# Optimization experiments

Hardware: AMD Instinct MI355X
Metric: run time of the kernel (lower is better)

Reference implementation:

```python
import jax, jax.numpy as jnp
import numpy as np

D_MODEL = 1024
NUM_HEADS = 16
D_K = D_MODEL // NUM_HEADS
TEMPERATURE = 1.0
EPS = 1e-6


def setup_inputs() -> dict:
    key = jax.random.key(0)
    ks = jax.random.split(key, 8)
    B, S, D, H = 2, 2048, D_MODEL, NUM_HEADS
    sc = 1.0 / np.sqrt(D)
    x = jax.random.normal(ks[0], (B, S, D), dtype=jnp.float32)
    Wq = jax.random.normal(ks[1], (D, D), dtype=jnp.float32) * sc
    Wk = jax.random.normal(ks[2], (D, D), dtype=jnp.float32) * sc
    Wv = jax.random.normal(ks[3], (D, D), dtype=jnp.float32) * sc
    Wo = jax.random.normal(ks[4], (D, D), dtype=jnp.float32) * sc
    bo = jnp.zeros((D,), dtype=jnp.float32)
    phase_scale = jnp.ones((H,), dtype=jnp.float32)
    # orthogonal init for entanglement matrix
    q, _ = np.linalg.qr(np.random.default_rng(0).normal(size=(H, H)))
    ent = jnp.asarray(q, dtype=jnp.float32)
    gamma = jnp.ones((D,), dtype=jnp.float32)
    beta = jnp.zeros((D,), dtype=jnp.float32)
    return {"x": x, "Wq": Wq, "Wk": Wk, "Wv": Wv, "Wo": Wo, "bo": bo,
            "phase_scale": phase_scale, "ent": ent, "gamma": gamma, "beta": beta}


def reference(x, Wq, Wk, Wv, Wo, bo, phase_scale, ent, gamma, beta):
    B, S, D = x.shape
    H, dk = NUM_HEADS, D_K
    # projections -> [B, H, S, dk]
    Q = (x @ Wq).reshape(B, S, H, dk).transpose(0, 2, 1, 3)
    K = (x @ Wk).reshape(B, S, H, dk).transpose(0, 2, 1, 3)
    V = (x @ Wv).reshape(B, S, H, dk).transpose(0, 2, 1, 3)
    # per-head QK^T, scaled, phase-modulated
    scores = jnp.einsum('bhqd,bhkd->bhqk', Q, K)
    inv = 1.0 / (float(np.sqrt(dk)) * TEMPERATURE)
    s = scores * (inv * phase_scale)[None, :, None, None]
    # real part of quantum phase: cos(s) + 0.1*cos(2s)  (imag part of V is zero,
    # so head_output = attended_real; the 0.1*attended_imag term vanishes)
    w = jnp.cos(s) + 0.1 * jnp.cos(2.0 * s)
    w = jax.nn.softmax(w, axis=-1)
    att = jnp.einsum('bhqk,bhkd->bhqd', w, V).transpose(0, 2, 1, 3)  # [B,S,H,dk]
    # faithful reproduction of tf.einsum('bsnd,hm->bsmd', ...): sums over n AND h
    att = jnp.einsum('bsnd,hm->bsmd', att, ent)
    out = att.reshape(B, S, D) @ Wo + bo
    r = out + x
    mu = jnp.mean(r, axis=-1, keepdims=True)
    var = jnp.mean(jnp.square(r - mu), axis=-1, keepdims=True)
    return gamma * (r - mu) * jax.lax.rsqrt(var + EPS) + beta
```

## Files before the change

### kernel.cpp

```cpp
#include <hip/hip_runtime.h>
#include <cstdint>
#include <cstddef>

#define S_LEN 2048
#define DMODEL 1024
#define NHEADS 16
#define DKH 64
#define MROWS 4096
#define BH_CNT 32

typedef __bf16 bf16x8 __attribute__((ext_vector_type(8)));
typedef __bf16 bf16x2 __attribute__((ext_vector_type(2)));
typedef float f32x4 __attribute__((ext_vector_type(4)));
typedef unsigned int u32;
typedef unsigned short u16;

__device__ __forceinline__ u16 f2bfu(float f) {
  u32 u = __float_as_uint(f);
  return (u16)((u + 0x7FFFu + ((u >> 16) & 1u)) >> 16);
}

__device__ __forceinline__ u32 pk_bf16(float a, float b) {
  bf16x2 v;
  v[0] = (__bf16)a;
  v[1] = (__bf16)b;
  return __builtin_bit_cast(u32, v);
}

__device__ __forceinline__ void gload16(void* lds, const void* g) {
  __builtin_amdgcn_global_load_lds(
      (const __attribute__((address_space(1))) void*)g,
      (__attribute__((address_space(3))) void*)lds, 16, 0, 0);
}

__global__ __launch_bounds__(256) void prep_xb_k(const float* __restrict__ x,
                                                 u16* __restrict__ xb) {
  int i = (blockIdx.x * 256 + threadIdx.x) * 4;
  float4 v = *(const float4*)(x + i);
  *(uint2*)(xb + i) = make_uint2(pk_bf16(v.x, v.y), pk_bf16(v.z, v.w));
}

__global__ __launch_bounds__(256) void prep_w_k(const float* __restrict__ Wq,
    const float* __restrict__ Wk, const float* __restrict__ Wv,
    const float* __restrict__ ps, u16* __restrict__ Wb) {
  __shared__ float tile[32][33];
  int sel = blockIdx.z;
  const float* W = sel == 0 ? Wq : (sel == 1 ? Wk : Wv);
  int k0 = blockIdx.x * 32, c0 = blockIdx.y * 32;
  int tx = threadIdx.x, ty = threadIdx.y;
#pragma unroll
  for (int i = 0; i < 4; ++i)
    tile[ty + i * 8][tx] = W[(size_t)(k0 + ty + i * 8) * DMODEL + c0 + tx];
  __syncthreads();
#pragma unroll
  for (int i = 0; i < 4; ++i) {
    int row = ty + i * 8;
    float v = tile[tx][row];
    if (sel == 1) v *= 0.019894367886486918f * ps[(c0 + row) >> 6];
    Wb[(size_t)(sel * 1024 + c0 + row) * DMODEL + k0 + tx] = f2bfu(v);
  }
}

__global__ __launch_bounds__(256) void prep_woeff_k(const float* __restrict__ Wo,
    const float* __restrict__ ent, float* __restrict__ Woeff) {
  __shared__ float e[16];
  int t = threadIdx.x;
  if (t < 16) {
    float s = 0.f;
#pragma unroll
    for (int h = 0; h < 16; ++h) s += ent[h * 16 + t];
    e[t] = s;
  }
  __syncthreads();
  int gid = blockIdx.x * 256 + t;
  int d = gid >> 10, j = gid & 1023;
  float acc = 0.f;
#pragma unroll
  for (int m = 0; m < 16; ++m) acc += e[m] * Wo[(size_t)((m << 6) + d) * DMODEL + j];
  Woeff[(size_t)d * DMODEL + j] = acc;
}

__global__ __launch_bounds__(256) void gemm_qkv_k(const u16* __restrict__ xb,
    const u16* __restrict__ Wb, u16* __restrict__ Qb, u16* __restrict__ Kb,
    u16* __restrict__ Vt) {
  __shared__ __align__(16) u16 SMEM[2][2][128 * 32];
  int tid = threadIdx.x;
  int lane = tid & 63, w = tid >> 6;
  int c = lane & 15, g = lane >> 4;
  int wr = w >> 1, wc = w & 1;
  int m0 = blockIdx.x * 128, n0 = blockIdx.y * 128;

  int cij0 = (w * 2) * 64 + lane, cij1 = (w * 2 + 1) * 64 + lane;
  int row0 = cij0 >> 2, kp0 = (cij0 & 3) ^ (row0 & 3);
  int row1 = cij1 >> 2, kp1 = (cij1 & 3) ^ (row1 & 3);
  const u16* a0p = xb + (size_t)(m0 + row0) * DMODEL + kp0 * 8;
  const u16* a1p = xb + (size_t)(m0 + row1) * DMODEL + kp1 * 8;
  const u16* b0p = Wb + (size_t)(n0 + row0) * DMODEL + kp0 * 8;
  const u16* b1p = Wb + (size_t)(n0 + row1) * DMODEL + kp1 * 8;

  f32x4 acc[4][4];
#pragma unroll
  for (int i = 0; i < 4; ++i)
#pragma unroll
    for (int j = 0; j < 4; ++j) acc[i][j] = (f32x4){0.f, 0.f, 0.f, 0.f};

  gload16(&SMEM[0][0][(w * 2) * 512], a0p);
  gload16(&SMEM[0][0][(w * 2 + 1) * 512], a1p);
  gload16(&SMEM[1][0][(w * 2) * 512], b0p);
  gload16(&SMEM[1][0][(w * 2 + 1) * 512], b1p);
  __syncthreads();

  int cur = 0;
  for (int kt = 0; kt < DMODEL; kt += 32) {
    if (kt + 32 < DMODEL) {
      int nx = cur ^ 1, ko = kt + 32;
      gload16(&SMEM[0][nx][(w * 2) * 512], a0p + ko);
      gload16(&SMEM[0][nx][(w * 2 + 1) * 512], a1p + ko);
      gload16(&SMEM[1][nx][(w * 2) * 512], b0p + ko);
      gload16(&SMEM[1][nx][(w * 2 + 1) * 512], b1p + ko);
    }
    const u16* Ac = SMEM[0][cur];
    const u16* Bc = SMEM[1][cur];
    bf16x8 af[4], bf[4];
#pragma unroll
    for (int i = 0; i < 4; ++i) {
      int ra = wr * 64 + i * 16 + c;
      af[i] = *(const bf16x8*)(Ac + ra * 32 + ((g ^ (ra & 3)) * 8));
      int rb = wc * 64 + i * 16 + c;
      bf[i] = *(const bf16x8*)(Bc + rb * 32 + ((g ^ (rb & 3)) * 8));
    }
#pragma unroll
    for (int i = 0; i < 4; ++i)
#pragma unroll
      for (int j = 0; j < 4; ++j)
        acc[i][j] = __builtin_amdgcn_mfma_f32_16x16x32_bf16(af[i], bf[j], acc[i][j], 0, 0, 0);
    __syncthreads();
    cur ^= 1;
  }

  int sel = n0 >> 10;
  char* Ls = (char*)&SMEM[0][0][0];
  if (sel == 2) {
#pragma unroll
    for (int i = 0; i < 4; ++i)
#pragma unroll
      for (int jf = 0; jf < 4; ++jf) {
        int n = wc * 64 + jf * 16 + c;
        int m = wr * 64 + i * 16 + 4 * g;
        int byte = n * 256 + ((m * 2) ^ ((n & 7) << 4));
        *(uint2*)(Ls + byte) = make_uint2(pk_bf16(acc[i][jf][0], acc[i][jf][1]),
                                          pk_bf16(acc[i][jf][2], acc[i][jf][3]));
      }
  } else {
#pragma unroll
    for (int i = 0; i < 4; ++i)
#pragma unroll
      for (int jf = 0; jf < 4; ++jf) {
        int n = wc * 64 + jf * 16 + c;
#pragma unroll
        for (int j = 0; j < 4; ++j) {
          int m = wr * 64 + i * 16 + 4 * g + j;
          int byte = m * 256 + ((n * 2) ^ ((m & 7) << 4));
          __bf16 hv = (__bf16)acc[i][jf][j];
          *(u16*)(Ls + byte) = __builtin_bit_cast(u16, hv);
        }
      }
  }
  __syncthreads();
  int r = tid >> 1, half = tid & 1;
  int h0 = (n0 & 1023) >> 6;
  int b = m0 >> 11, sbase = m0 & 2047;
  u16* dst;
  if (sel == 2) {
    int bh = b * 16 + h0 + (r >> 6), d = r & 63;
    dst = Vt + ((size_t)bh * DKH + d) * S_LEN + sbase + half * 64;
  } else {
    u16* base = (sel == 0 ? Qb : Kb);
    int bh = b * 16 + h0 + half;
    dst = base + ((size_t)bh * S_LEN + sbase + r) * DKH;
  }
#pragma unroll
  for (int kk = 0; kk < 8; ++kk) {
    int byte = r * 256 + ((half * 128 + kk * 16) ^ ((r & 7) << 4));
    *(uint4*)(dst + kk * 8) = *(const uint4*)(Ls + byte);
  }
}

__global__ __launch_bounds__(256) void attn_k(const u16* __restrict__ Qb,
    const u16* __restrict__ Kb, const u16* __restrict__ Vt,
    float* __restrict__ attbuf) {
  __shared__ __align__(16) u16 Ks[2][64 * 64];
  __shared__ __align__(16) u16 Vs[2][64 * 64];
  __shared__ __align__(16) u32 Ps[4 * 16 * 32];
  int fid = blockIdx.x;
  int swz = (fid & 7) * 128 + (fid >> 3);
  int bh = swz >> 5, qblk = swz & 31;
  int tid = threadIdx.x;
  int lane = tid & 63, w = tid >> 6;
  int c = lane & 15, g = lane >> 4;
  int q0 = qblk * 64 + w * 16;
  const u16* Kbase = Kb + (size_t)bh * S_LEN * DKH;
  const u16* Vbase = Vt + (size_t)bh * DKH * S_LEN;

  int cij0 = (w * 2) * 64 + lane, cij1 = (w * 2 + 1) * 64 + lane;
  int srow0 = cij0 >> 3, skp0 = (cij0 & 7) ^ (srow0 & 7);
  int srow1 = cij1 >> 3, skp1 = (cij1 & 7) ^ (srow1 & 7);
  const u16* k0p = Kbase + (size_t)srow0 * DKH + skp0 * 8;
  const u16* k1p = Kbase + (size_t)srow1 * DKH + skp1 * 8;
  const u16* v0p = Vbase + (size_t)srow0 * S_LEN + skp0 * 8;
  const u16* v1p = Vbase + (size_t)srow1 * S_LEN + skp1 * 8;

  gload16(&Ks[0][(w * 2) * 512], k0p);
  gload16(&Ks[0][(w * 2 + 1) * 512], k1p);
  gload16(&Vs[0][(w * 2) * 512], v0p);
  gload16(&Vs[0][(w * 2 + 1) * 512], v1p);

  bf16x8 qf0, qf1;
  {
    const u16* qp = Qb + ((size_t)bh * S_LEN + q0 + c) * DKH + g * 8;
    qf0 = *(const bf16x8*)qp;
    qf1 = *(const bf16x8*)(qp + 32);
  }
  f32x4 attT[4];
#pragma unroll
  for (int i = 0; i < 4; ++i) attT[i] = (f32x4){0.f, 0.f, 0.f, 0.f};
  float dacc0 = 0.f, dacc1 = 0.f;
  u32* Pw = Ps + w * 512;
  int wAddr[4];
#pragma unroll
  for (int fm = 0; fm < 4; ++fm) {
    int kr0 = fm * 16 + 4 * g;
    int ch = (kr0 >> 3) ^ (c & 7);
    wAddr[fm] = c * 32 + ch * 4 + ((kr0 & 7) >> 1);
  }
  const float L2E = 1.4426950408889634f;

  auto compute = [&](const u16* Kc, const u16* Vc) {
    f32x4 sT[4];
    __builtin_amdgcn_s_setprio(1);
#pragma unroll
    for (int fm = 0; fm < 4; ++fm) {
      int row = fm * 16 + c;
      bf16x8 a0 = *(const bf16x8*)(Kc + row * 64 + ((g ^ (row & 7)) * 8));
      bf16x8 a1 = *(const bf16x8*)(Kc + row * 64 + (((4 + g) ^ (row & 7)) * 8));
      f32x4 z = (f32x4){0.f, 0.f, 0.f, 0.f};
      z = __builtin_amdgcn_mfma_f32_16x16x32_bf16(a0, qf0, z, 0, 0, 0);
      z = __builtin_amdgcn_mfma_f32_16x16x32_bf16(a1, qf1, z, 0, 0, 0);
      sT[fm] = z;
    }
    __builtin_amdgcn_s_setprio(0);
#pragma unroll
    for (int fm = 0; fm < 4; ++fm) {
      float pv[4];
#pragma unroll
      for (int j = 0; j < 4; ++j) {
        float cv = __builtin_amdgcn_cosf(sT[fm][j]);
        float w2 = __fmaf_rn(cv, __fmaf_rn(0.2f * L2E, cv, L2E), -0.1f * L2E);
        pv[j] = __builtin_amdgcn_exp2f(w2);
      }
      dacc0 += pv[0] + pv[1];
      dacc1 += pv[2] + pv[3];
      *(uint2*)(Pw + wAddr[fm]) = make_uint2(pk_bf16(pv[0], pv[1]), pk_bf16(pv[2], pv[3]));
    }
    __builtin_amdgcn_s_setprio(1);
#pragma unroll
    for (int bb = 0; bb < 2; ++bb) {
      bf16x8 pf = *(const bf16x8*)(Pw + c * 32 + (((4 * bb + g) ^ (c & 7)) * 4));
#pragma unroll
      for (int fd = 0; fd < 4; ++fd) {
        int row = fd * 16 + c;
        bf16x8 vf = *(const bf16x8*)(Vc + row * 64 + ((((4 * bb + g) ^ (row & 7))) * 8));
        attT[fd] = __builtin_amdgcn_mfma_f32_16x16x32_bf16(vf, pf, attT[fd], 0, 0, 0);
      }
    }
    __builtin_amdgcn_s_setprio(0);
  };

  const u16* kc0 = k0p;
  const u16* kc1 = k1p;
  const u16* vc0 = v0p;
  const u16* vc1 = v1p;
  __syncthreads();
  for (int kt = 0; kt < S_LEN; kt += 128) {
    kc0 += 64 * DKH; kc1 += 64 * DKH; vc0 += 64; vc1 += 64;
    gload16(&Ks[1][(w * 2) * 512], kc0);
    gload16(&Ks[1][(w * 2 + 1) * 512], kc1);
    gload16(&Vs[1][(w * 2) * 512], vc0);
    gload16(&Vs[1][(w * 2 + 1) * 512], vc1);
    compute(Ks[0], Vs[0]);
    __syncthreads();
    if (kt + 128 < S_LEN) {
      kc0 += 64 * DKH; kc1 += 64 * DKH; vc0 += 64; vc1 += 64;
      gload16(&Ks[0][(w * 2) * 512], kc0);
      gload16(&Ks[0][(w * 2 + 1) * 512], kc1);
      gload16(&Vs[0][(w * 2) * 512], vc0);
      gload16(&Vs[0][(w * 2 + 1) * 512], vc1);
    }
    compute(Ks[1], Vs[1]);
    __syncthreads();
  }
  float dacc = dacc0 + dacc1;
  dacc += __shfl_xor(dacc, 16, 64);
  dacc += __shfl_xor(dacc, 32, 64);
  float inv = 1.f / dacc;
  float* ob = attbuf + ((size_t)bh * S_LEN + q0 + c) * DKH;
#pragma unroll
  for (int fd = 0; fd < 4; ++fd) {
    float4 ov;
    ov.x = attT[fd][0] * inv;
    ov.y = attT[fd][1] * inv;
    ov.z = attT[fd][2] * inv;
    ov.w = attT[fd][3] * inv;
    *(float4*)(ob + fd * 16 + 4 * g) = ov;
  }
}

__global__ __launch_bounds__(256) void fuse_out_ln_k(const float* __restrict__ attbuf,
    const float* __restrict__ Woeff, const float* __restrict__ bo,
    const float* __restrict__ x, const float* __restrict__ gamma,
    const float* __restrict__ beta, float* __restrict__ out) {
  __shared__ float red[8][256];
  __shared__ __align__(16) float a[8][64];
  __shared__ float sred[8][4][2];
  int t = threadIdx.x;
  int r0 = blockIdx.x * 8;
  int d = t & 63, hg = t >> 6;
#pragma unroll
  for (int rr = 0; rr < 8; ++rr) {
    int m = r0 + rr, b = m >> 11, sr = m & 2047;
    float pa = 0.f;
#pragma unroll
    for (int hh = 0; hh < 4; ++hh) {
      int h = hg * 4 + hh;
      pa += attbuf[(((size_t)(b * 16 + h)) * S_LEN + sr) * DKH + d];
    }
    red[rr][t] = pa;
  }
  __syncthreads();
#pragma unroll
  for (int e = 0; e < 2; ++e) {
    int idx = t + e * 256;
    int rr = idx >> 6, dd = idx & 63;
    a[rr][dd] = red[rr][dd] + red[rr][64 + dd] + red[rr][128 + dd] + red[rr][192 + dd];
  }
  __syncthreads();

  float o[8][4];
#pragma unroll
  for (int rr = 0; rr < 8; ++rr) { o[rr][0] = o[rr][1] = o[rr][2] = o[rr][3] = 0.f; }
  int c4 = t * 4;
  for (int dd = 0; dd < 64; dd += 4) {
    float4 wv0 = *(const float4*)(Woeff + (size_t)(dd + 0) * DMODEL + c4);
    float4 wv1 = *(const float4*)(Woeff + (size_t)(dd + 1) * DMODEL + c4);
    float4 wv2 = *(const float4*)(Woeff + (size_t)(dd + 2) * DMODEL + c4);
    float4 wv3 = *(const float4*)(Woeff + (size_t)(dd + 3) * DMODEL + c4);
#pragma unroll
    for (int rr = 0; rr < 8; ++rr) {
      float4 av = *(const float4*)&a[rr][dd];
      o[rr][0] += av.x * wv0.x + av.y * wv1.x + av.z * wv2.x + av.w * wv3.x;
      o[rr][1] += av.x * wv0.y + av.y * wv1.y + av.z * wv2.y + av.w * wv3.y;
      o[rr][2] += av.x * wv0.z + av.y * wv1.z + av.z * wv2.z + av.w * wv3.z;
      o[rr][3] += av.x * wv0.w + av.y * wv1.w + av.z * wv2.w + av.w * wv3.w;
    }
  }
  float4 bv = *(const float4*)(bo + c4);
  int w = t >> 6, lane = t & 63;
#pragma unroll
  for (int rr = 0; rr < 8; ++rr) {
    int m = r0 + rr;
    float4 xv = *(const float4*)(x + (size_t)m * DMODEL + c4);
    o[rr][0] += bv.x + xv.x;
    o[rr][1] += bv.y + xv.y;
    o[rr][2] += bv.z + xv.z;
    o[rr][3] += bv.w + xv.w;
    float s = o[rr][0] + o[rr][1] + o[rr][2] + o[rr][3];
    float q = o[rr][0] * o[rr][0] + o[rr][1] * o[rr][1] + o[rr][2] * o[rr][2] + o[rr][3] * o[rr][3];
#pragma unroll
    for (int mm = 1; mm < 64; mm <<= 1) {
      s += __shfl_xor(s, mm, 64);
      q += __shfl_xor(q, mm, 64);
    }
    if (lane == 0) { sred[rr][w][0] = s; sred[rr][w][1] = q; }
  }
  __syncthreads();
  float4 gv = *(const float4*)(gamma + c4);
  float4 bev = *(const float4*)(beta + c4);
#pragma unroll
  for (int rr = 0; rr < 8; ++rr) {
    float s = sred[rr][0][0] + sred[rr][1][0] + sred[rr][2][0] + sred[rr][3][0];
    float q = sred[rr][0][1] + sred[rr][1][1] + sred[rr][2][1] + sred[rr][3][1];
    float mu = s * (1.f / 1024.f);
    float var = q * (1.f / 1024.f) - mu * mu;
    float rs = rsqrtf(var + 1e-6f);
    int m = r0 + rr;
    float4 ov;
    ov.x = gv.x * (o[rr][0] - mu) * rs + bev.x;
    ov.y = gv.y * (o[rr][1] - mu) * rs + bev.y;
    ov.z = gv.z * (o[rr][2] - mu) * rs + bev.z;
    ov.w = gv.w * (o[rr][3] - mu) * rs + bev.w;
    *(float4*)(out + (size_t)m * DMODEL + c4) = ov;
  }
}

extern "C" void kernel_launch(void* const* d_in, const int* in_sizes, int n_in,
                              void* d_out, int out_size, void* d_ws, size_t ws_size,
                              hipStream_t stream) {
  const float* x = (const float*)d_in[0];
  const float* Wq = (const float*)d_in[1];
  const float* Wk = (const float*)d_in[2];
  const float* Wv = (const float*)d_in[3];
  const float* Wo = (const float*)d_in[4];
  const float* bo = (const float*)d_in[5];
  const float* ps = (const float*)d_in[6];
  const float* ent = (const float*)d_in[7];
  const float* gamma = (const float*)d_in[8];
  const float* beta = (const float*)d_in[9];
  float* out = (float*)d_out;

  char* ws = (char*)d_ws;
  size_t o = 0;
  u16* xb = (u16*)(ws + o);    o += (size_t)MROWS * DMODEL * 2;
  u16* Wb = (u16*)(ws + o);    o += (size_t)3072 * 1024 * 2;
  u16* Qb = (u16*)(ws + o);    o += (size_t)BH_CNT * S_LEN * DKH * 2;
  u16* Kb = (u16*)(ws + o);    o += (size_t)BH_CNT * S_LEN * DKH * 2;
  u16* Vt = (u16*)(ws + o);    o += (size_t)BH_CNT * S_LEN * DKH * 2;
  float* Woeff = (float*)(ws + o);  o += (size_t)DKH * DMODEL * 4;
  float* attbuf = (float*)(ws + o); o += (size_t)BH_CNT * S_LEN * DKH * 4;

  prep_xb_k<<<dim3(4096), dim3(256), 0, stream>>>(x, xb);
  prep_w_k<<<dim3(32, 32, 3), dim3(32, 8), 0, stream>>>(Wq, Wk, Wv, ps, Wb);
  prep_woeff_k<<<dim3(256), dim3(256), 0, stream>>>(Wo, ent, Woeff);
  gemm_qkv_k<<<dim3(32, 24), dim3(256), 0, stream>>>(xb, Wb, Qb, Kb, Vt);
  attn_k<<<dim3(1024), dim3(256), 0, stream>>>(Qb, Kb, Vt, attbuf);
  fuse_out_ln_k<<<dim3(512), dim3(256), 0, stream>>>(attbuf, Woeff, bo, x, gamma, beta, out);
}
```

Baseline: 139.1 us.

## Split attention keys across waves and pass P via permlane swaps instead of LDS

The attention kernel's work split changes: each wave now handles 32 queries and half of each 64-key tile instead of 16 queries and the full tile. The P matrix is rearranged into the MFMA B-operand layout in registers with permlane32/permlane16 swaps rather than a round-trip through LDS. Partial outputs and softmax denominators from the two key-halves are combined through LDS at the end. This removes the per-tile LDS write/read of P and reuses each K/V fragment across two query groups, at the cost of more registers and a final cross-wave reduction.

```diff
diff --git a/kernel.cpp b/kernel.cpp
--- a/kernel.cpp
+++ b/kernel.cpp
@@ -12,6 +12,7 @@
 typedef __bf16 bf16x8 __attribute__((ext_vector_type(8)));
 typedef __bf16 bf16x2 __attribute__((ext_vector_type(2)));
 typedef float f32x4 __attribute__((ext_vector_type(4)));
+typedef unsigned int u32x4 __attribute__((ext_vector_type(4)));
 typedef unsigned int u32;
 typedef unsigned short u16;
 
@@ -25,6 +26,23 @@
   v[0] = (__bf16)a;
   v[1] = (__bf16)b;
   return __builtin_bit_cast(u32, v);
+}
+
+__device__ __forceinline__ void pl32swap(u32& a, u32& b) {
+#if __has_builtin(__builtin_amdgcn_permlane32_swap)
+  auto r = __builtin_amdgcn_permlane32_swap((int)a, (int)b, false, false);
+  a = (u32)r[0]; b = (u32)r[1];
+#else
+  asm volatile("v_permlane32_swap_b32 %0, %1" : "+v"(a), "+v"(b));
+#endif
+}
+__device__ __forceinline__ void pl16swap(u32& a, u32& b) {
+#if __has_builtin(__builtin_amdgcn_permlane16_swap)
+  auto r = __builtin_amdgcn_permlane16_swap((int)a, (int)b, false, false);
+  a = (u32)r[0]; b = (u32)r[1];
+#else
+  asm volatile("v_permlane16_swap_b32 %0, %1" : "+v"(a), "+v"(b));
+#endif
 }
 
 __device__ __forceinline__ void gload16(void* lds, const void* g) {
@@ -191,14 +209,15 @@
     float* __restrict__ attbuf) {
   __shared__ __align__(16) u16 Ks[2][64 * 64];
   __shared__ __align__(16) u16 Vs[2][64 * 64];
-  __shared__ __align__(16) u32 Ps[4 * 16 * 32];
+  __shared__ float dred[4][2][16];
   int fid = blockIdx.x;
   int swz = (fid & 7) * 128 + (fid >> 3);
   int bh = swz >> 5, qblk = swz & 31;
   int tid = threadIdx.x;
   int lane = tid & 63, w = tid >> 6;
   int c = lane & 15, g = lane >> 4;
-  int q0 = qblk * 64 + w * 16;
+  int h = w >> 1, qh = w & 1;
+  int q0 = qblk * 64;
   const u16* Kbase = Kb + (size_t)bh * S_LEN * DKH;
   const u16* Vbase = Vt + (size_t)bh * DKH * S_LEN;
 
@@ -215,63 +234,72 @@
   gload16(&Vs[0][(w * 2) * 512], v0p);
   gload16(&Vs[0][(w * 2 + 1) * 512], v1p);
 
-  bf16x8 qf0, qf1;
-  {
-    const u16* qp = Qb + ((size_t)bh * S_LEN + q0 + c) * DKH + g * 8;
-    qf0 = *(const bf16x8*)qp;
-    qf1 = *(const bf16x8*)(qp + 32);
-  }
-  f32x4 attT[4];
-#pragma unroll
-  for (int i = 0; i < 4; ++i) attT[i] = (f32x4){0.f, 0.f, 0.f, 0.f};
-  float dacc0 = 0.f, dacc1 = 0.f;
-  u32* Pw = Ps + w * 512;
-  int wAddr[4];
-#pragma unroll
-  for (int fm = 0; fm < 4; ++fm) {
-    int kr0 = fm * 16 + 4 * g;
-    int ch = (kr0 >> 3) ^ (c & 7);
-    wAddr[fm] = c * 32 + ch * 4 + ((kr0 & 7) >> 1);
-  }
+  bf16x8 qf[2][2];
+#pragma unroll
+  for (int qg = 0; qg < 2; ++qg) {
+    const u16* qp = Qb + ((size_t)bh * S_LEN + q0 + qh * 32 + qg * 16 + c) * DKH + g * 8;
+    qf[qg][0] = *(const bf16x8*)qp;
+    qf[qg][1] = *(const bf16x8*)(qp + 32);
+  }
+  f32x4 attT[4][2];
+#pragma unroll
+  for (int i = 0; i < 4; ++i)
+#pragma unroll
+    for (int qg = 0; qg < 2; ++qg) attT[i][qg] = (f32x4){0.f, 0.f, 0.f, 0.f};
+  float dacc[2] = {0.f, 0.f};
   const float L2E = 1.4426950408889634f;
 
   auto compute = [&](const u16* Kc, const u16* Vc) {
-    f32x4 sT[4];
+    f32x4 sT[2][2];
     __builtin_amdgcn_s_setprio(1);
 #pragma unroll
-    for (int fm = 0; fm < 4; ++fm) {
-      int row = fm * 16 + c;
+    for (int fm = 0; fm < 2; ++fm) {
+      int row = h * 32 + fm * 16 + c;
       bf16x8 a0 = *(const bf16x8*)(Kc + row * 64 + ((g ^ (row & 7)) * 8));
       bf16x8 a1 = *(const bf16x8*)(Kc + row * 64 + (((4 + g) ^ (row & 7)) * 8));
-      f32x4 z = (f32x4){0.f, 0.f, 0.f, 0.f};
-      z = __builtin_amdgcn_mfma_f32_16x16x32_bf16(a0, qf0, z, 0, 0, 0);
-      z = __builtin_amdgcn_mfma_f32_16x16x32_bf16(a1, qf1, z, 0, 0, 0);
-      sT[fm] = z;
+#pragma unroll
+      for (int qg = 0; qg < 2; ++qg) {
+        f32x4 z = (f32x4){0.f, 0.f, 0.f, 0.f};
+        z = __builtin_amdgcn_mfma_f32_16x16x32_bf16(a0, qf[qg][0], z, 0, 0, 0);
+        sT[fm][qg] = __builtin_amdgcn_mfma_f32_16x16x32_bf16(a1, qf[qg][1], z, 0, 0, 0);
+      }
     }
     __builtin_amdgcn_s_setprio(0);
-#pragma unroll
-    for (int fm = 0; fm < 4; ++fm) {
-      float pv[4];
-#pragma unroll
-      for (int j = 0; j < 4; ++j) {
-        float cv = __builtin_amdgcn_cosf(sT[fm][j]);
-        float w2 = __fmaf_rn(cv, __fmaf_rn(0.2f * L2E, cv, L2E), -0.1f * L2E);
-        pv[j] = __builtin_amdgcn_exp2f(w2);
+    u32 wq[2][2][2];
+#pragma unroll
+    for (int fm = 0; fm < 2; ++fm)
+#pragma unroll
+      for (int qg = 0; qg < 2; ++qg) {
+        float pv[4];
+#pragma unroll
+        for (int j = 0; j < 4; ++j) {
+          float cv = __builtin_amdgcn_cosf(sT[fm][qg][j]);
+          float w2 = __fmaf_rn(cv, __fmaf_rn(0.2f * L2E, cv, L2E), -0.1f * L2E);
+          pv[j] = __builtin_amdgcn_exp2f(w2);
+        }
+        dacc[qg] += (pv[0] + pv[1]) + (pv[2] + pv[3]);
+        wq[qg][fm][0] = pk_bf16(pv[0], pv[1]);
+        wq[qg][fm][1] = pk_bf16(pv[2], pv[3]);
       }
-      dacc0 += pv[0] + pv[1];
-      dacc1 += pv[2] + pv[3];
-      *(uint2*)(Pw + wAddr[fm]) = make_uint2(pk_bf16(pv[0], pv[1]), pk_bf16(pv[2], pv[3]));
+    bf16x8 pf[2];
+#pragma unroll
+    for (int qg = 0; qg < 2; ++qg) {
+      u32 b0 = wq[qg][0][0], b2 = wq[qg][1][0];
+      pl32swap(b0, b2);
+      pl16swap(b0, b2);
+      u32 b1 = wq[qg][0][1], b3 = wq[qg][1][1];
+      pl32swap(b1, b3);
+      pl16swap(b1, b3);
+      pf[qg] = __builtin_bit_cast(bf16x8, (u32x4){b0, b1, b2, b3});
     }
     __builtin_amdgcn_s_setprio(1);
 #pragma unroll
-    for (int bb = 0; bb < 2; ++bb) {
-      bf16x8 pf = *(const bf16x8*)(Pw + c * 32 + (((4 * bb + g) ^ (c & 7)) * 4));
-#pragma unroll
-      for (int fd = 0; fd < 4; ++fd) {
-        int row = fd * 16 + c;
-        bf16x8 vf = *(const bf16x8*)(Vc + row * 64 + ((((4 * bb + g) ^ (row & 7))) * 8));
-        attT[fd] = __builtin_amdgcn_mfma_f32_16x16x32_bf16(vf, pf, attT[fd], 0, 0, 0);
-      }
+    for (int fd = 0; fd < 4; ++fd) {
+      int vrow = fd * 16 + c;
+      bf16x8 vf = *(const bf16x8*)(Vc + vrow * 64 + (((4 * h + g) ^ (vrow & 7)) * 8));
+#pragma unroll
+      for (int qg = 0; qg < 2; ++qg)
+        attT[fd][qg] = __builtin_amdgcn_mfma_f32_16x16x32_bf16(vf, pf[qg], attT[fd][qg], 0, 0, 0);
     }
     __builtin_amdgcn_s_setprio(0);
   };
@@ -299,19 +327,41 @@
     compute(Ks[1], Vs[1]);
     __syncthreads();
   }
-  float dacc = dacc0 + dacc1;
-  dacc += __shfl_xor(dacc, 16, 64);
-  dacc += __shfl_xor(dacc, 32, 64);
-  float inv = 1.f / dacc;
-  float* ob = attbuf + ((size_t)bh * S_LEN + q0 + c) * DKH;
-#pragma unroll
-  for (int fd = 0; fd < 4; ++fd) {
-    float4 ov;
-    ov.x = attT[fd][0] * inv;
-    ov.y = attT[fd][1] * inv;
-    ov.z = attT[fd][2] * inv;
-    ov.w = attT[fd][3] * inv;
-    *(float4*)(ob + fd * 16 + 4 * g) = ov;
+
+#pragma unroll
+  for (int qg = 0; qg < 2; ++qg) {
+    dacc[qg] += __shfl_xor(dacc[qg], 16, 64);
+    dacc[qg] += __shfl_xor(dacc[qg], 32, 64);
+  }
+  if (g == 0) {
+    dred[w][0][c] = dacc[0];
+    dred[w][1][c] = dacc[1];
+  }
+  float* R = (float*)&Ks[0][0];
+  if (h == 1) {
+    float* Rq = R + qh * 2048;
+#pragma unroll
+    for (int fd = 0; fd < 4; ++fd)
+#pragma unroll
+      for (int qg = 0; qg < 2; ++qg)
+        *(f32x4*)&Rq[(qg * 16 + c) * 64 + fd * 16 + 4 * g] = attT[fd][qg];
+  }
+  __syncthreads();
+  if (h == 0) {
+    float inv[2];
+#pragma unroll
+    for (int qg = 0; qg < 2; ++qg)
+      inv[qg] = 1.f / (dred[w][qg][c] + dred[w ^ 2][qg][c]);
+    float* Rq = R + qh * 2048;
+#pragma unroll
+    for (int fd = 0; fd < 4; ++fd)
+#pragma unroll
+      for (int qg = 0; qg < 2; ++qg) {
+        f32x4 part = *(const f32x4*)&Rq[(qg * 16 + c) * 64 + fd * 16 + 4 * g];
+        f32x4 tot = (attT[fd][qg] + part) * inv[qg];
+        int q = q0 + qh * 32 + qg * 16 + c;
+        *(f32x4*)(attbuf + ((size_t)bh * S_LEN + q) * DKH + fd * 16 + 4 * g) = tot;
+      }
   }
 }
 
```

Result: slower. 143.4 us (+3.1%).
